# Optimization experiments

Measured on AMD Instinct MI355X. Metric: run time of the kernel, lower is better.

The kernel has to match this reference:

```python
import jax, jax.numpy as jnp
import numpy as np

B, S, C = 16, 1024, 8
V, D, E, H, R = 50257, 512, 8, 512, 32
F, RT, CD, Q = 1024, 512, 64, 128
EPS = 1e-6


def _normalize(x):
    n = jnp.maximum(jnp.linalg.norm(x, axis=-1, keepdims=True), EPS)
    return x / n


def _fake_quantize(x):
    # F.normalize then straight-through int8 quant on the unit vector
    xn = _normalize(x)
    q = jnp.clip(jnp.round(xn * 127.0), -127.0, 127.0)
    return xn + jax.lax.stop_gradient(q / 127.0 - xn)


def setup_inputs() -> dict:
    key = jax.random.key(0)
    ks = iter(jax.random.split(key, 64))

    def w(shape, s=0.02):
        return (jax.random.normal(next(ks), shape, dtype=jnp.float32) * s)

    inp = {}
    inp['prefix_tokens'] = jax.random.randint(next(ks), (B, S), 0, V, dtype=jnp.int32)
    inp['chunk_inputs'] = jax.random.randint(next(ks), (B, C), 0, V, dtype=jnp.int32)
    inp['chunk_targets'] = jax.random.randint(next(ks), (B, C), 0, V, dtype=jnp.int32)
    inp['next_chunk_tokens'] = jax.random.randint(next(ks), (B, C), 0, V, dtype=jnp.int32)

    inp['emb'] = w((V, D))
    # stacked per-expert AffineExpert params
    inp['Wa'] = w((E, D, H)); inp['ba'] = jnp.zeros((E, H), jnp.float32)
    inp['Wg'] = w((E, D, R)); inp['bg'] = jnp.zeros((E, R), jnp.float32)
    inp['Wu'] = w((E, D, H)); inp['bu'] = jnp.zeros((E, H), jnp.float32)
    inp['u_mat'] = w((E, H, R)); inp['v_mat'] = w((E, H, R))
    inp['Wp'] = w((E, H, F)); inp['bp'] = jnp.zeros((E, F), jnp.float32)
    # gate MLP
    inp['Wg1'] = w((D, D)); inp['bg1'] = jnp.zeros((D,), jnp.float32)
    inp['Wg2'] = w((D, E)); inp['bg2'] = jnp.zeros((E,), jnp.float32)
    # query / target / key / code-expansion / write-code
    inp['Wq'] = w((F, Q)); inp['bq'] = jnp.zeros((Q,), jnp.float32)
    inp['Wt1'] = w((2 * D, RT)); inp['bt1'] = jnp.zeros((RT,), jnp.float32)
    inp['Wt2'] = w((RT, RT)); inp['bt2'] = jnp.zeros((RT,), jnp.float32)
    inp['Wk'] = w((RT, Q)); inp['bk'] = jnp.zeros((Q,), jnp.float32)
    inp['Web'] = w((CD, RT))  # expansion_basis (no bias)
    inp['Wwc'] = w((F, CD)); inp['bwc'] = jnp.zeros((CD,), jnp.float32)
    # ctx MLP
    inp['Wc1'] = w((2 * F, F)); inp['bc1'] = jnp.zeros((F,), jnp.float32)
    inp['Wc2'] = w((F, F)); inp['bc2'] = jnp.zeros((F,), jnp.float32)
    # chunk decoder
    inp['chunk_pos'] = w((C, F))
    inp['Wci'] = w((D + F, F)); inp['bci'] = jnp.zeros((F,), jnp.float32)
    inp['Wm1'] = w((F, F)); inp['bm1'] = jnp.zeros((F,), jnp.float32)
    inp['Wm2'] = w((F, F)); inp['bm2'] = jnp.zeros((F,), jnp.float32)
    inp['Wlm'] = w((F, V)); inp['blm'] = jnp.zeros((V,), jnp.float32)
    return inp


def _expert_scan(x, Wa, ba, Wg, bg, Wu, bu, u_mat, v_mat):
    # x: [B,S,D]; precompute all per-step projections as one big GEMM each,
    # leading axis = time for lax.scan. A,U: [S,E,B,H], G: [S,E,B,R]
    A = jax.nn.sigmoid(jnp.einsum('bsd,edh->sebh', x, Wa) + ba[None, :, None, :])
    G = jnp.einsum('bsd,edr->sebr', x, Wg) + bg[None, :, None, :]
    U = jnp.einsum('bsd,edh->sebh', x, Wu) + bu[None, :, None, :]

    def step(state, inp):  # state: [E,B,H]
        a, g, u = inp
        low = jnp.einsum('ebh,ehr->ebr', state, v_mat) * g
        state = a * state + u + jnp.einsum('ebr,ehr->ebh', low, u_mat)
        return state, None

    state0 = jnp.zeros((E, B, H), x.dtype)
    state, _ = jax.lax.scan(step, state0, (A, G, U))
    return state  # [E,B,H]


def reference(prefix_tokens, chunk_inputs, chunk_targets, next_chunk_tokens,
              emb, Wa, ba, Wg, bg, Wu, bu, u_mat, v_mat, Wp, bp,
              Wg1, bg1, Wg2, bg2, Wq, bq, Wt1, bt1, Wt2, bt2, Wk, bk,
              Web, Wwc, bwc, Wc1, bc1, Wc2, bc2,
              chunk_pos, Wci, bci, Wm1, bm1, Wm2, bm2, Wlm, blm):
    # ---- encode_prefix ----
    prefix_emb = emb[prefix_tokens]                       # [B,S,D]
    summary = prefix_emb.mean(axis=1)                     # [B,D]
    gate_probs = jax.nn.softmax(jax.nn.silu(summary @ Wg1 + bg1) @ Wg2 + bg2, axis=-1)  # [B,E]
    states = _expert_scan(prefix_emb, Wa, ba, Wg, bg, Wu, bu, u_mat, v_mat)             # [E,B,H]
    proj = jnp.einsum('ebh,ehf->ebf', states, Wp) + bp[:, None, :]                       # [E,B,F]
    fused = jnp.einsum('ebf,be->bf', proj, gate_probs)    # [B,F]

    # ---- query / target / key ----
    q_st = _fake_quantize(fused @ Wq + bq)                # [B,Q]
    chunk_emb = emb[chunk_targets].mean(axis=1)           # [B,D]
    next_emb = emb[next_chunk_tokens].mean(axis=1)        # [B,D]
    t_in = jnp.concatenate([chunk_emb, next_emb], axis=-1)
    target_state = _normalize(jax.nn.silu(t_in @ Wt1 + bt1) @ Wt2 + bt2)  # [B,RT]
    target_k_st = _fake_quantize(target_state @ Wk + bk)  # [B,Q]

    # ---- read_context (bank=None path -> zero read) ----
    zero_read = jnp.zeros_like(fused)
    c_in = jnp.concatenate([fused, zero_read], axis=-1)
    ctx = jax.nn.silu(c_in @ Wc1 + bc1) @ Wc2 + bc2       # [B,F]

    # ---- write_from_ctx ----
    write_codes = ctx @ Wwc + bwc                         # [B,CD]
    write_state = _normalize(write_codes @ Web)           # [B,RT]
    write_k_st = _fake_quantize(write_state @ Wk + bk)    # [B,Q]

    # ---- decode_chunk ----
    tok = emb[chunk_inputs]                               # [B,C,D]
    ctx_rep = jnp.broadcast_to(ctx[:, None, :], (B, C, F))
    hidden = jnp.concatenate([tok, ctx_rep], axis=-1) @ Wci + bci + chunk_pos[None]  # [B,C,F]
    hidden = jax.nn.silu(hidden @ Wm1 + bm1) @ Wm2 + bm2
    logits = hidden @ Wlm + blm                           # [B,C,V]

    # ---- losses ----
    logp = jax.nn.log_softmax(logits, axis=-1)
    token_loss = -jnp.take_along_axis(logp, chunk_targets[..., None], axis=-1)[..., 0]
    loss_nll = token_loss.mean()
    sim = (q_st @ target_k_st.T) / jnp.sqrt(jnp.float32(Q))  # [B,B]
    return logits, loss_nll, sim, write_k_st
```

## Files before the change

### kernel.cpp

```cpp
#include <hip/hip_runtime.h>
#include <math.h>

constexpr int BB = 16;
constexpr int SS = 1024;
constexpr int CC = 8;
constexpr int VV = 50257;
constexpr int DD = 512;
constexpr int EE = 8;
constexpr int HH = 512;
constexpr int RR = 32;
constexpr int FF = 1024;
constexpr int RTd = 512;
constexpr int CDd = 64;
constexpr int QQ = 128;
constexpr int SCH = 128;

typedef short bf16x8 __attribute__((ext_vector_type(8)));
typedef float f32x4 __attribute__((ext_vector_type(4)));

__device__ __forceinline__ float sigm(float x){ return 1.0f/(1.0f+expf(-x)); }

__device__ __forceinline__ unsigned short f2bf(float f){
  unsigned int u = __float_as_uint(f);
  u += 0x7fff + ((u>>16)&1);
  return (unsigned short)(u>>16);
}
__device__ __forceinline__ float bf2f(unsigned short h){
  return __uint_as_float(((unsigned int)h)<<16);
}

__device__ __forceinline__ void gload16(unsigned short* l, const unsigned short* g){
  __builtin_amdgcn_global_load_lds(
      (const __attribute__((address_space(1))) unsigned int*)(g),
      (__attribute__((address_space(3))) unsigned int*)(l), 16, 0, 0);
}

__global__ __launch_bounds__(256) void gather_split(const int* __restrict__ toks,
    const float* __restrict__ emb,
    unsigned short* __restrict__ xh, unsigned short* __restrict__ xl){
  int idx = blockIdx.x*256 + threadIdx.x;
  int row = idx >> 7;
  int c4  = idx & 127;
  float4 v = ((const float4*)emb)[(size_t)toks[row]*128 + c4];
  float vv[4] = {v.x, v.y, v.z, v.w};
  ushort4 h, l;
  unsigned short hh[4], ll[4];
  #pragma unroll
  for (int j=0;j<4;j++){
    hh[j] = f2bf(vv[j]);
    ll[j] = f2bf(vv[j] - bf2f(hh[j]));
  }
  h = make_ushort4(hh[0],hh[1],hh[2],hh[3]);
  l = make_ushort4(ll[0],ll[1],ll[2],ll[3]);
  ((ushort4*)xh)[idx] = h;
  ((ushort4*)xl)[idx] = l;
}

__global__ __launch_bounds__(512) void colsum_part(const unsigned short* __restrict__ xh,
    const unsigned short* __restrict__ xl, float* __restrict__ part){
  int b = blockIdx.y, j = blockIdx.x, d = threadIdx.x;
  float s = 0.f;
  for (int k=0;k<64;k++){
    size_t idx = ((size_t)(b*SS) + j*64 + k)*DD + d;
    s += bf2f(xh[idx]) + bf2f(xl[idx]);
  }
  part[(b*16 + j)*DD + d] = s;
}
__global__ __launch_bounds__(512) void colsum_final(const float* __restrict__ part,
                                                    float* __restrict__ summary){
  int b = blockIdx.x, d = threadIdx.x;
  float s = 0.f;
  for (int j=0;j<16;j++) s += part[(b*16 + j)*DD + d];
  summary[b*DD + d] = s * (1.0f/1024.0f);
}

__global__ __launch_bounds__(128) void gate_h1(const float* __restrict__ summary,
                                               const float* __restrict__ Wg1,
                                               const float* __restrict__ bg1,
                                               float* __restrict__ h1){
  int t = threadIdx.x; int j = blockIdx.x*128 + t;
  __shared__ float sm[16*512];
  for (int idx=t; idx<8192; idx+=128) sm[idx] = summary[idx];
  __syncthreads();
  float acc[16] = {0};
  for (int d=0; d<DD; d++){
    float w = Wg1[d*DD + j];
    #pragma unroll
    for (int b2=0;b2<16;b2++) acc[b2] += sm[b2*DD + d]*w;
  }
  #pragma unroll
  for (int b2=0;b2<16;b2++){ float v = acc[b2] + bg1[j]; h1[b2*DD + j] = v*sigm(v); }
}
__global__ __launch_bounds__(128) void gate_probs_k(const float* __restrict__ h1,
                                                    const float* __restrict__ Wg2,
                                                    const float* __restrict__ bg2,
                                                    float* __restrict__ gate){
  int t = threadIdx.x;
  int b = t>>3, e = t&7;
  float acc = bg2[e];
  for (int d=0; d<DD; d++) acc += h1[b*DD + d]*Wg2[d*EE + e];
  __shared__ float lg[16][8];
  lg[b][e] = acc;
  __syncthreads();
  if (e==0){
    float m = -3.4e38f;
    for (int i=0;i<8;i++) m = fmaxf(m, lg[b][i]);
    float s = 0.f; float ex[8];
    for (int i=0;i<8;i++){ ex[i] = expf(lg[b][i]-m); s += ex[i]; }
    for (int i=0;i<8;i++) gate[b*EE + i] = ex[i]/s;
  }
}

__global__ __launch_bounds__(256) void convT_wl(const float* __restrict__ Wa,
    const float* __restrict__ Wu,
    unsigned short* __restrict__ WaTh, unsigned short* __restrict__ WaTl,
    unsigned short* __restrict__ WuTh, unsigned short* __restrict__ WuTl){
  int ez = blockIdx.z;
  const float* W; unsigned short *Th, *Tl;
  if (ez < 8){
    W = Wa + (size_t)ez*DD*HH; Th = WaTh + (size_t)ez*HH*DD; Tl = WaTl + (size_t)ez*HH*DD;
  } else {
    int e2 = ez-8;
    W = Wu + (size_t)e2*DD*HH; Th = WuTh + (size_t)e2*HH*DD; Tl = WuTl + (size_t)e2*HH*DD;
  }
  int k0 = blockIdx.x*64, c0 = blockIdx.y*64;
  __shared__ float tile[64][65];
  int t = threadIdx.x;
  for (int i=0;i<16;i++){
    int id = t + i*256;
    int cc = id&63, kk = id>>6;
    tile[kk][cc] = W[(size_t)(k0+kk)*HH + c0+cc];
  }
  __syncthreads();
  for (int i=0;i<16;i++){
    int id = t + i*256;
    int kk = id&63, cc = id>>6;
    float f = tile[kk][cc];
    unsigned short h = f2bf(f);
    float lo = f - bf2f(h);
    Th[(size_t)(c0+cc)*DD + k0+kk] = h;
    Tl[(size_t)(c0+cc)*DD + k0+kk] = f2bf(lo);
  }
}
__global__ __launch_bounds__(256) void convT_g(const float* __restrict__ Wge,
    unsigned short* __restrict__ WgeTh, unsigned short* __restrict__ WgeTl){
  int k0 = blockIdx.x*64, e = blockIdx.y;
  __shared__ float tile[64][33];
  int t = threadIdx.x;
  for (int i=0;i<8;i++){
    int id = t + i*256;
    int r = id&31, kk = id>>5;
    tile[kk][r] = Wge[((size_t)e*DD + k0+kk)*RR + r];
  }
  __syncthreads();
  for (int i=0;i<8;i++){
    int id = t + i*256;
    int kk = id&63, r = id>>6;
    float f = tile[kk][r];
    unsigned short h = f2bf(f);
    float lo = f - bf2f(h);
    WgeTh[(size_t)(e*RR + r)*DD + k0+kk] = h;
    WgeTl[(size_t)(e*RR + r)*DD + k0+kk] = f2bf(lo);
  }
}

__global__ __launch_bounds__(512, 4) void aug_scan(
    const unsigned short* __restrict__ xh, const unsigned short* __restrict__ xl,
    const unsigned short* __restrict__ WaTh, const unsigned short* __restrict__ WaTl,
    const unsigned short* __restrict__ WuTh, const unsigned short* __restrict__ WuTl,
    const unsigned short* __restrict__ WgeTh, const unsigned short* __restrict__ WgeTl,
    const float* __restrict__ ba, const float* __restrict__ bu, const float* __restrict__ bge,
    float* __restrict__ Aw, float* __restrict__ Uw, float* __restrict__ Gw,
    const float* __restrict__ Ar, const float* __restrict__ Ur, const float* __restrict__ Gr,
    const float* __restrict__ v_mat, const float* __restrict__ u_mat,
    float* __restrict__ states,
    int s0, int do_aug, int do_scan)
{
  __shared__ __align__(16) unsigned short lds[32768];
  const int t = threadIdx.x;

  if (blockIdx.x < 128){
    if (!do_scan) return;
    const int e = blockIdx.x >> 4;
    const int b = blockIdx.x & 15;
    const int r = t & 31, grp = t >> 5;
    float* stf   = (float*)lds;
    float* partf = (float*)lds + 1024;
    float* lowf  = (float*)lds + 1312;
    float vreg[32];
    #pragma unroll
    for (int i=0;i<32;i++) vreg[i] = v_mat[((size_t)e*HH + grp*32 + i)*RR + r];
    float ureg[32];
    {
      const float4* up = (const float4*)(u_mat + ((size_t)e*HH + t)*RR);
      #pragma unroll
      for (int j=0;j<8;j++){
        float4 v4 = up[j];
        ureg[j*4+0]=v4.x; ureg[j*4+1]=v4.y; ureg[j*4+2]=v4.z; ureg[j*4+3]=v4.w;
      }
    }
    const size_t base  = ((size_t)e*BB + b)*HH + t;
    const size_t gbase = ((size_t)e*BB + b)*RR + r;
    const size_t strAU = (size_t)EE*BB*HH;
    const size_t strG  = (size_t)EE*BB*RR;
    float streg = states[base];
    stf[t] = streg;
    float a0 = Ar[base], u0 = Ur[base];
    float g0 = (t < 32) ? Gr[gbase] : 0.f;
    float a1 = 0.f, u1 = 0.f, g1 = 0.f;
    a1 = Ar[base + strAU]; u1 = Ur[base + strAU];
    g1 = (t < 32) ? Gr[gbase + strG] : 0.f;
    __syncthreads();
    int cur = 0;
    for (int s=0; s<SCH; s++){
      float a2 = 0.f, u2 = 0.f, g2 = 0.f;
      if (s+2 < SCH){
        a2 = Ar[base + (size_t)(s+2)*strAU];
        u2 = Ur[base + (size_t)(s+2)*strAU];
        if (t < 32) g2 = Gr[gbase + (size_t)(s+2)*strG];
      }
      float p = 0.f;
      #pragma unroll
      for (int i=0;i<32;i++) p += stf[cur*512 + grp*32+i]*vreg[i];
      p += __shfl_xor(p, 32, 64);
      if ((t & 32) == 0) partf[r*9 + (grp>>1)] = p;
      __syncthreads();
      if (t < 32){
        float ss2 = 0.f;
        #pragma unroll
        for (int j=0;j<8;j++) ss2 += partf[t*9 + j];
        lowf[t] = ss2 * g0;
      }
      __syncthreads();
      float acc2 = 0.f;
      #pragma unroll
      for (int i=0;i<32;i++) acc2 += lowf[i]*ureg[i];
      streg = a0*streg + u0 + acc2;
      stf[(cur^1)*512 + t] = streg;
      cur ^= 1;
      a0=a1; u0=u1; g0=g1; a1=a2; u1=u2; g1=g2;
      __syncthreads();
    }
    states[base] = streg;
    return;
  }

  if (!do_aug) return;
  const int aid = blockIdx.x - 128;
  const int b  = aid & 15;
  const int ct = aid >> 4;
  const bool isG = (ct >= 64);
  const int lane = t & 63, wv = t >> 6;

  unsigned short* const XSH = lds;
  unsigned short* const XSL = lds + 8192;
  unsigned short* const WAH = lds + 16384;
  unsigned short* const WAL = lds + 20480;
  unsigned short* const WUH = lds + 24576;
  unsigned short* const WUL = lds + 28672;

  int e = 0, c0 = 0;
  const unsigned short* Wptr[4];
  if (!isG){
    e = ct >> 3; c0 = (ct & 7)*64;
    Wptr[0] = WaTh + ((size_t)e*HH + c0)*DD;
    Wptr[1] = WaTl + ((size_t)e*HH + c0)*DD;
    Wptr[2] = WuTh + ((size_t)e*HH + c0)*DD;
    Wptr[3] = WuTl + ((size_t)e*HH + c0)*DD;
  } else {
    c0 = (ct - 64)*64;
    Wptr[0] = WgeTh + (size_t)c0*DD;
    Wptr[1] = WgeTl + (size_t)c0*DD;
    Wptr[2] = Wptr[0]; Wptr[3] = Wptr[1];
  }
  unsigned short* const LW[4] = {WAH, WAL, WUH, WUL};
  const unsigned short* xhp = xh + ((size_t)b*SS + s0)*DD;
  const unsigned short* xlp = xl + ((size_t)b*SS + s0)*DD;

  f32x4 acc[2][4] = {};

#define STAGE(J, K0) { \
    const int wbase = (J)*512 + (t & 448); \
    const int id = wbase + lane; \
    if ((J) < 4){ \
      const int local = id & 1023; \
      const int row = local >> 3; \
      const int kq = (local & 7) ^ (row & 7); \
      const unsigned short* g = (((J) < 2) ? xhp : xlp) + (size_t)row*DD + (K0) + kq*8; \
      unsigned short* lp = (((J) < 2) ? XSH : XSL) + (wbase & 1023)*8; \
      gload16(lp, g); \
    } else { \
      const int local = id & 511; \
      const int kq = local >> 6; \
      const int c = (local & 63) ^ kq; \
      const unsigned short* g = Wptr[(J)-4] + (size_t)c*DD + (K0) + kq*8; \
      unsigned short* lp = LW[(J)-4] + (wbase & 511)*8; \
      gload16(lp, g); \
    } }

  const int strip = wv & 3;
  const int mode  = wv >> 2;
  unsigned short* const WH = mode ? WUH : WAH;
  unsigned short* const WL = mode ? WUL : WAL;

  for (int kc=0; kc<8; kc++){
    const int k0 = kc*64;
    if (kc) __syncthreads();
    STAGE(0, k0) STAGE(1, k0) STAGE(2, k0) STAGE(3, k0)
    STAGE(4, k0) STAGE(5, k0)
    if (!isG){ STAGE(6, k0) STAGE(7, k0) }
    __syncthreads();

    if (!isG){
      #pragma unroll
      for (int ks=0; ks<2; ks++){
        const int kq4 = ks*4 + (lane>>4);
        const int rr0 = strip*32 + (lane&15);
        const int rr1 = rr0 + 16;
        bf16x8 ah0 = *(const bf16x8*)&XSH[(rr0*8 + (kq4^(rr0&7)))*8];
        bf16x8 ah1 = *(const bf16x8*)&XSH[(rr1*8 + (kq4^(rr1&7)))*8];
        bf16x8 al0 = *(const bf16x8*)&XSL[(rr0*8 + (kq4^(rr0&7)))*8];
        bf16x8 al1 = *(const bf16x8*)&XSL[(rr1*8 + (kq4^(rr1&7)))*8];
        #pragma unroll
        for (int cf=0; cf<4; cf++){
          const int cc = cf*16 + (lane&15);
          bf16x8 bh = *(const bf16x8*)&WH[(kq4*64 + (cc^kq4))*8];
          bf16x8 bl = *(const bf16x8*)&WL[(kq4*64 + (cc^kq4))*8];
          acc[0][cf] = __builtin_amdgcn_mfma_f32_16x16x32_bf16(ah0, bh, acc[0][cf], 0,0,0);
          acc[0][cf] = __builtin_amdgcn_mfma_f32_16x16x32_bf16(ah0, bl, acc[0][cf], 0,0,0);
          acc[0][cf] = __builtin_amdgcn_mfma_f32_16x16x32_bf16(al0, bh, acc[0][cf], 0,0,0);
          acc[1][cf] = __builtin_amdgcn_mfma_f32_16x16x32_bf16(ah1, bh, acc[1][cf], 0,0,0);
          acc[1][cf] = __builtin_amdgcn_mfma_f32_16x16x32_bf16(ah1, bl, acc[1][cf], 0,0,0);
          acc[1][cf] = __builtin_amdgcn_mfma_f32_16x16x32_bf16(al1, bh, acc[1][cf], 0,0,0);
        }
      }
    } else {
      #pragma unroll
      for (int ks=0; ks<2; ks++){
        const int kq4 = ks*4 + (lane>>4);
        const int rr0 = wv*16 + (lane&15);
        bf16x8 ah0 = *(const bf16x8*)&XSH[(rr0*8 + (kq4^(rr0&7)))*8];
        bf16x8 al0 = *(const bf16x8*)&XSL[(rr0*8 + (kq4^(rr0&7)))*8];
        #pragma unroll
        for (int cf=0; cf<4; cf++){
          const int cc = cf*16 + (lane&15);
          bf16x8 bh = *(const bf16x8*)&WAH[(kq4*64 + (cc^kq4))*8];
          bf16x8 bl = *(const bf16x8*)&WAL[(kq4*64 + (cc^kq4))*8];
          acc[0][cf] = __builtin_amdgcn_mfma_f32_16x16x32_bf16(ah0, bh, acc[0][cf], 0,0,0);
          acc[0][cf] = __builtin_amdgcn_mfma_f32_16x16x32_bf16(ah0, bl, acc[0][cf], 0,0,0);
          acc[0][cf] = __builtin_amdgcn_mfma_f32_16x16x32_bf16(al0, bh, acc[0][cf], 0,0,0);
        }
      }
    }
  }
#undef STAGE

  const int cl = lane & 15;
  const int r4 = (lane >> 4) * 4;
  if (!isG){
    #pragma unroll
    for (int rf=0; rf<2; rf++){
      #pragma unroll
      for (int cf=0; cf<4; cf++){
        #pragma unroll
        for (int i=0;i<4;i++){
          int sl = strip*32 + rf*16 + r4 + i;
          int ce = c0 + cf*16 + cl;
          float v = acc[rf][cf][i];
          if (mode == 0){
            v += ba[e*HH + ce];
            v = sigm(v);
            Aw[((size_t)(sl*EE + e)*BB + b)*HH + ce] = v;
          } else {
            v += bu[e*HH + ce];
            Uw[((size_t)(sl*EE + e)*BB + b)*HH + ce] = v;
          }
        }
      }
    }
  } else {
    #pragma unroll
    for (int cf=0; cf<4; cf++){
      #pragma unroll
      for (int i=0;i<4;i++){
        int sl = wv*16 + r4 + i;
        int g = c0 + cf*16 + cl;
        int ee = g >> 5, r2 = g & 31;
        float v = acc[0][cf][i] + bge[ee*RR + r2];
        Gw[((size_t)(sl*EE + ee)*BB + b)*RR + r2] = v;
      }
    }
  }
}

__global__ __launch_bounds__(128) void proj_partial(const float* __restrict__ states,
    const float* __restrict__ Wp, const float* __restrict__ gate, float* __restrict__ pf){
  int fc = blockIdx.x, e = blockIdx.y, t = threadIdx.x;
  __shared__ float stl[16*512];
  for (int idx=t; idx<8192; idx+=128) stl[idx] = states[(size_t)e*8192 + idx];
  __syncthreads();
  int f = fc*128 + t;
  float acc[16] = {0};
  for (int h=0; h<HH; h++){
    float w = Wp[((size_t)e*HH + h)*FF + f];
    #pragma unroll
    for (int b2=0;b2<16;b2++) acc[b2] += stl[b2*HH + h]*w;
  }
  #pragma unroll
  for (int b2=0;b2<16;b2++) pf[((size_t)(e*16 + b2))*FF + f] = gate[b2*EE + e]*acc[b2];
}
__global__ __launch_bounds__(256) void fuse_reduce(const float* __restrict__ pf,
    const float* __restrict__ gate, const float* __restrict__ bp, float* __restrict__ fused){
  int idx = blockIdx.x*256 + threadIdx.x;
  int b = idx >> 10, f = idx & 1023;
  float s = 0.f;
  #pragma unroll
  for (int e=0;e<8;e++) s += pf[((size_t)(e*16 + b))*FF + f] + gate[b*EE + e]*bp[e*FF + f];
  fused[idx] = s;
}

__global__ __launch_bounds__(128) void fq_linear(const float* __restrict__ in, int Kin,
    const float* __restrict__ W, const float* __restrict__ bias, float* __restrict__ out){
  int b = blockIdx.x, t = threadIdx.x;
  __shared__ float xin[1024];
  __shared__ float red[2];
  for (int k=t;k<Kin;k+=128) xin[k] = in[(size_t)b*Kin + k];
  __syncthreads();
  float acc = bias[t];
  for (int k=0;k<Kin;k++) acc += xin[k]*W[k*QQ + t];
  float ss = acc*acc;
  #pragma unroll
  for (int off=32; off; off>>=1) ss += __shfl_xor(ss, off, 64);
  if ((t&63)==0) red[t>>6] = ss;
  __syncthreads();
  float n = fmaxf(sqrtf(red[0]+red[1]), 1e-6f);
  float xn = acc / n;
  float q = fminf(fmaxf(rintf(xn*127.0f), -127.0f), 127.0f) * (1.0f/127.0f);
  out[b*QQ + t] = q;
}

__global__ __launch_bounds__(512) void chunk_means(const int* __restrict__ ct,
    const int* __restrict__ nct, const float* __restrict__ emb, float* __restrict__ tin){
  int b = blockIdx.x, d = threadIdx.x;
  float ce=0.f, ne=0.f;
  for (int c=0;c<CC;c++){
    ce += emb[(size_t)ct[b*CC+c]*DD + d];
    ne += emb[(size_t)nct[b*CC+c]*DD + d];
  }
  tin[b*1024 + d] = ce*0.125f;
  tin[b*1024 + 512 + d] = ne*0.125f;
}

__global__ __launch_bounds__(512) void target_state_kernel(const float* __restrict__ tin,
    const float* __restrict__ Wt1, const float* __restrict__ bt1,
    const float* __restrict__ Wt2, const float* __restrict__ bt2, float* __restrict__ outts){
  int b = blockIdx.x, t = threadIdx.x;
  __shared__ float xin[1024];
  __shared__ float h1[512];
  __shared__ float red[8];
  for (int k=t;k<1024;k+=512) xin[k] = tin[b*1024 + k];
  __syncthreads();
  float acc = bt1[t];
  for (int k=0;k<1024;k++) acc += xin[k]*Wt1[k*RTd + t];
  acc = acc*sigm(acc);
  h1[t] = acc;
  __syncthreads();
  float y = bt2[t];
  for (int k=0;k<512;k++) y += h1[k]*Wt2[k*RTd + t];
  float ss = y*y;
// ... 205 lines not shown
  #pragma unroll
  for (int off=32; off; off>>=1){
    float m2 = __shfl_xor(m, off, 64);
    float s2 = __shfl_xor(s, off, 64);
    float mn = fmaxf(m, m2);
    s = s*expf(m - mn) + s2*expf(m2 - mn);
    m = mn;
  }
  __shared__ float ms[8], ssh[8];
  if ((t&63)==0){ ms[t>>6] = m; ssh[t>>6] = s; }
  __syncthreads();
  if (t==0){
    float M = ms[0], S = ssh[0];
    for (int i=1;i<8;i++){
      float mn = fmaxf(M, ms[i]);
      S = S*expf(M-mn) + ssh[i]*expf(ms[i]-mn);
      M = mn;
    }
    tl[row] = M + logf(S) - p[tgt[row]];
  }
}
__global__ __launch_bounds__(128) void loss_reduce(const float* __restrict__ tl,
                                                   float* __restrict__ out){
  int t = threadIdx.x;
  float v = tl[t];
  #pragma unroll
  for (int off=32; off; off>>=1) v += __shfl_xor(v, off, 64);
  __shared__ float r2[2];
  if ((t&63)==0) r2[t>>6] = v;
  __syncthreads();
  if (t==0) out[0] = (r2[0]+r2[1]) * (1.0f/128.0f);
}

extern "C" void kernel_launch(void* const* d_in, const int* in_sizes, int n_in,
                              void* d_out, int out_size, void* d_ws, size_t ws_size,
                              hipStream_t stream){
  (void)in_sizes; (void)n_in; (void)out_size;
  const int*  prefix = (const int*)d_in[0];
  const int*  cinp   = (const int*)d_in[1];
  const int*  ctgt   = (const int*)d_in[2];
  const int*  nctk   = (const int*)d_in[3];
  const float* emb  = (const float*)d_in[4];
  const float* Wa   = (const float*)d_in[5];
  const float* ba   = (const float*)d_in[6];
  const float* Wge  = (const float*)d_in[7];
  const float* bge  = (const float*)d_in[8];
  const float* Wu   = (const float*)d_in[9];
  const float* bu   = (const float*)d_in[10];
  const float* u_mat= (const float*)d_in[11];
  const float* v_mat= (const float*)d_in[12];
  const float* Wp   = (const float*)d_in[13];
  const float* bp   = (const float*)d_in[14];
  const float* Wg1  = (const float*)d_in[15];
  const float* bg1  = (const float*)d_in[16];
  const float* Wg2  = (const float*)d_in[17];
  const float* bg2  = (const float*)d_in[18];
  const float* Wq   = (const float*)d_in[19];
  const float* bq   = (const float*)d_in[20];
  const float* Wt1  = (const float*)d_in[21];
  const float* bt1  = (const float*)d_in[22];
  const float* Wt2  = (const float*)d_in[23];
  const float* bt2  = (const float*)d_in[24];
  const float* Wk   = (const float*)d_in[25];
  const float* bk   = (const float*)d_in[26];
  const float* Web  = (const float*)d_in[27];
  const float* Wwc  = (const float*)d_in[28];
  const float* bwc  = (const float*)d_in[29];
  const float* Wc1  = (const float*)d_in[30];
  const float* bc1  = (const float*)d_in[31];
  const float* Wc2  = (const float*)d_in[32];
  const float* bc2  = (const float*)d_in[33];
  const float* cpos = (const float*)d_in[34];
  const float* Wci  = (const float*)d_in[35];
  const float* bci  = (const float*)d_in[36];
  const float* Wm1  = (const float*)d_in[37];
  const float* bm1  = (const float*)d_in[38];
  const float* Wm2  = (const float*)d_in[39];
  const float* bm2  = (const float*)d_in[40];
  const float* Wlm  = (const float*)d_in[41];
  const float* blm  = (const float*)d_in[42];

  float* ws = (float*)d_ws;
  size_t off = 0;
  unsigned short* xh_all = (unsigned short*)(ws + off); off += (size_t)BB*SS*DD/2;
  unsigned short* xl_all = (unsigned short*)(ws + off); off += (size_t)BB*SS*DD/2;
  float* Abuf0  = ws + off; off += (size_t)SCH*EE*BB*HH;
  float* Ubuf0  = ws + off; off += (size_t)SCH*EE*BB*HH;
  float* Gbuf0  = ws + off; off += (size_t)SCH*EE*BB*RR;
  float* statesb= ws + off; off += (size_t)EE*BB*HH;
  float* partb  = ws + off; off += (size_t)BB*16*DD;
  float* summb  = ws + off; off += (size_t)BB*DD;
  float* h1b    = ws + off; off += (size_t)BB*DD;
  float* gateb  = ws + off; off += (size_t)BB*EE;
  float* pfb    = ws + off; off += (size_t)EE*BB*FF;
  float* fusedb = ws + off; off += (size_t)BB*FF;
  float* qstb   = ws + off; off += (size_t)BB*QQ;
  float* tinb   = ws + off; off += (size_t)BB*2*DD;
  float* tstb   = ws + off; off += (size_t)BB*RTd;
  float* tkb    = ws + off; off += (size_t)BB*QQ;
  float* ctxb   = ws + off; off += (size_t)BB*FF;
  float* hctxb  = ws + off; off += (size_t)BB*FF;
  float* wsnb   = ws + off; off += (size_t)BB*RTd;
  float* xcatb  = ws + off; off += (size_t)BB*CC*(DD+FF);
  float* hid1b  = ws + off; off += (size_t)BB*CC*FF;
  float* h2b    = ws + off; off += (size_t)BB*CC*FF;
  float* hidb   = ws + off; off += (size_t)BB*CC*FF;
  float* tlb    = ws + off; off += (size_t)BB*CC;
  float* ppart  = ws + off; off += (size_t)4*BB*CC*FF;
  unsigned short* WaTh = (unsigned short*)(ws + off); off += (size_t)EE*DD*HH/2;
  unsigned short* WaTl = (unsigned short*)(ws + off); off += (size_t)EE*DD*HH/2;
  unsigned short* WuTh = (unsigned short*)(ws + off); off += (size_t)EE*DD*HH/2;
  unsigned short* WuTl = (unsigned short*)(ws + off); off += (size_t)EE*DD*HH/2;
  unsigned short* WgeTh= (unsigned short*)(ws + off); off += (size_t)EE*DD*RR/2;
  unsigned short* WgeTl= (unsigned short*)(ws + off); off += (size_t)EE*DD*RR/2;
  unsigned short* hhb  = (unsigned short*)(ws + off); off += (size_t)BB*CC*FF/2;
  unsigned short* hlb  = (unsigned short*)(ws + off); off += (size_t)BB*CC*FF/2;
  float* Abuf1  = ws + off; off += (size_t)SCH*EE*BB*HH;
  float* Ubuf1  = ws + off; off += (size_t)SCH*EE*BB*HH;
  float* Gbuf1  = ws + off; off += (size_t)SCH*EE*BB*RR;
  const bool fused = ws_size >= off * sizeof(float);

  float* out = (float*)d_out;
  const size_t LOGITS_OFF = 0;
  const size_t LOSS_OFF = (size_t)BB*CC*VV;
  const size_t SIM_OFF  = LOSS_OFF + 1;
  const size_t WK_OFF   = SIM_OFF + (size_t)BB*BB;

  convT_wl<<<dim3(8,8,16), 256, 0, stream>>>(Wa, Wu, WaTh, WaTl, WuTh, WuTl);
  convT_g<<<dim3(8,8), 256, 0, stream>>>(Wge, WgeTh, WgeTl);

  gather_split<<<8192, 256, 0, stream>>>(prefix, emb, xh_all, xl_all);
  colsum_part<<<dim3(16,16), 512, 0, stream>>>(xh_all, xl_all, partb);
  colsum_final<<<16, 512, 0, stream>>>(partb, summb);
  gate_h1<<<4, 128, 0, stream>>>(summb, Wg1, bg1, h1b);
  gate_probs_k<<<1, 128, 0, stream>>>(h1b, Wg2, bg2, gateb);

  hipMemsetAsync(statesb, 0, (size_t)EE*BB*HH*sizeof(float), stream);

  if (fused){
    for (int c=0; c<=8; c++){
      int da = (c<8) ? 1 : 0;
      int dscn = (c>=1) ? 1 : 0;
      float* Aw = (c&1) ? Abuf1 : Abuf0;
      float* Uw = (c&1) ? Ubuf1 : Ubuf0;
      float* Gw = (c&1) ? Gbuf1 : Gbuf0;
      const float* Ar = ((c-1)&1) ? Abuf1 : Abuf0;
      const float* Ur = ((c-1)&1) ? Ubuf1 : Ubuf0;
      const float* Gr = ((c-1)&1) ? Gbuf1 : Gbuf0;
      int grid = da ? 1216 : 128;
      aug_scan<<<grid, 512, 0, stream>>>(xh_all, xl_all,
          WaTh, WaTl, WuTh, WuTl, WgeTh, WgeTl, ba, bu, bge,
          Aw, Uw, Gw, Ar, Ur, Gr, v_mat, u_mat, statesb,
          c*SCH, da, dscn);
    }
  } else {
    for (int c=0; c<8; c++){
      aug_scan<<<1216, 512, 0, stream>>>(xh_all, xl_all,
          WaTh, WaTl, WuTh, WuTl, WgeTh, WgeTl, ba, bu, bge,
          Abuf0, Ubuf0, Gbuf0, Abuf0, Ubuf0, Gbuf0, v_mat, u_mat, statesb,
          c*SCH, 1, 0);
      aug_scan<<<128, 512, 0, stream>>>(xh_all, xl_all,
          WaTh, WaTl, WuTh, WuTl, WgeTh, WgeTl, ba, bu, bge,
          Abuf0, Ubuf0, Gbuf0, Abuf0, Ubuf0, Gbuf0, v_mat, u_mat, statesb,
          c*SCH, 0, 1);
    }
  }

  proj_partial<<<dim3(8,8), 128, 0, stream>>>(statesb, Wp, gateb, pfb);
  fuse_reduce<<<64, 256, 0, stream>>>(pfb, gateb, bp, fusedb);

  fq_linear<<<16, 128, 0, stream>>>(fusedb, FF, Wq, bq, qstb);
  chunk_means<<<16, 512, 0, stream>>>(ctgt, nctk, emb, tinb);
  target_state_kernel<<<16, 512, 0, stream>>>(tinb, Wt1, bt1, Wt2, bt2, tstb);
  fq_linear<<<16, 128, 0, stream>>>(tstb, RTd, Wk, bk, tkb);

  gemm_part<<<dim3(16,1,4), 256, 0, stream>>>(fusedb, Wc1, ppart, FF, 4, 16);
  gemm_combine<<<64, 256, 0, stream>>>(ppart, bc1, nullptr, hctxb, 4, 16, 1);
  gemm_part<<<dim3(16,1,4), 256, 0, stream>>>(hctxb, Wc2, ppart, FF, 4, 16);
  gemm_combine<<<64, 256, 0, stream>>>(ppart, bc2, nullptr, ctxb, 4, 16, 0);

  write_state_kernel<<<16, 512, 0, stream>>>(ctxb, Wwc, bwc, Web, wsnb);
  fq_linear<<<16, 128, 0, stream>>>(wsnb, RTd, Wk, bk, out + WK_OFF);
  sim_kernel<<<1, 256, 0, stream>>>(qstb, tkb, out + SIM_OFF);

  build_xcat<<<768, 256, 0, stream>>>(cinp, emb, ctxb, xcatb);
  gemm_part<<<dim3(16,8,4), 256, 0, stream>>>(xcatb, Wci, ppart, DD+FF, 4, 128);
  gemm_combine<<<512, 256, 0, stream>>>(ppart, bci, cpos, hid1b, 4, 128, 0);
  gemm_part<<<dim3(16,8,4), 256, 0, stream>>>(hid1b, Wm1, ppart, FF, 4, 128);
  gemm_combine<<<512, 256, 0, stream>>>(ppart, bm1, nullptr, h2b, 4, 128, 1);
  gemm_part<<<dim3(16,8,4), 256, 0, stream>>>(h2b, Wm2, ppart, FF, 4, 128);
  gemm_combine<<<512, 256, 0, stream>>>(ppart, bm2, nullptr, hidb, 4, 128, 0);

  split_h<<<512, 256, 0, stream>>>(hidb, hhb, hlb);
  logits_mfma<<<(VV+63)/64, 256, 0, stream>>>(hhb, hlb, Wlm, blm, out + LOGITS_OFF);

  softmax_nll<<<BB*CC, 512, 0, stream>>>(out + LOGITS_OFF, ctgt, tlb);
  loss_reduce<<<1, 128, 0, stream>>>(tlb, out + LOSS_OFF);
}
```

Before: 1.818 ms.

## Pre-pack activations and weights into MFMA tile order with double-buffered LDS staging

After: 1.611 ms (median of 3 runs). 11.4% less time.

```diff
diff --git a/kernel.cpp b/kernel.cpp
--- a/kernel.cpp
+++ b/kernel.cpp
@@ -35,34 +35,39 @@
       (__attribute__((address_space(3))) unsigned int*)(l), 16, 0, 0);
 }
 
-__global__ __launch_bounds__(256) void gather_split(const int* __restrict__ toks,
-    const float* __restrict__ emb,
-    unsigned short* __restrict__ xh, unsigned short* __restrict__ xl){
-  int idx = blockIdx.x*256 + threadIdx.x;
-  int row = idx >> 7;
-  int c4  = idx & 127;
-  float4 v = ((const float4*)emb)[(size_t)toks[row]*128 + c4];
-  float vv[4] = {v.x, v.y, v.z, v.w};
-  ushort4 h, l;
-  unsigned short hh[4], ll[4];
-  #pragma unroll
-  for (int j=0;j<4;j++){
-    hh[j] = f2bf(vv[j]);
-    ll[j] = f2bf(vv[j] - bf2f(hh[j]));
-  }
-  h = make_ushort4(hh[0],hh[1],hh[2],hh[3]);
-  l = make_ushort4(ll[0],ll[1],ll[2],ll[3]);
-  ((ushort4*)xh)[idx] = h;
-  ((ushort4*)xl)[idx] = l;
-}
-
-__global__ __launch_bounds__(512) void colsum_part(const unsigned short* __restrict__ xh,
-    const unsigned short* __restrict__ xl, float* __restrict__ part){
+__global__ __launch_bounds__(256) void gather_pack(const int* __restrict__ toks,
+    const float* __restrict__ emb, unsigned short* __restrict__ xp){
+  int id = blockIdx.x*256 + threadIdx.x;
+  int b = id >> 17;
+  int rem = id & 131071;
+  int c = rem >> 14;
+  int rem2 = rem & 16383;
+  int kc = rem2 >> 10;
+  int pb = rem2 & 1023;
+  int row = pb >> 3, q = pb & 7;
+  int v = q ^ (row & 7);
+  int kq = v >> 1, h = v & 1;
+  int tok = toks[b*SS + c*128 + row];
+  const float* src = emb + (size_t)tok*DD + kc*32 + kq*8;
+  unsigned short o[8];
+  #pragma unroll
+  for (int j=0;j<8;j++){
+    float f = src[j];
+    unsigned short hi = f2bf(f);
+    o[j] = h ? f2bf(f - bf2f(hi)) : hi;
+  }
+  ushort4* dst = (ushort4*)(xp + (size_t)id*8);
+  dst[0] = make_ushort4(o[0],o[1],o[2],o[3]);
+  dst[1] = make_ushort4(o[4],o[5],o[6],o[7]);
+}
+
+__global__ __launch_bounds__(512) void colsum_part(const int* __restrict__ toks,
+    const float* __restrict__ emb, float* __restrict__ part){
   int b = blockIdx.y, j = blockIdx.x, d = threadIdx.x;
   float s = 0.f;
   for (int k=0;k<64;k++){
-    size_t idx = ((size_t)(b*SS) + j*64 + k)*DD + d;
-    s += bf2f(xh[idx]) + bf2f(xl[idx]);
+    int tok = toks[b*SS + j*64 + k];
+    s += emb[(size_t)tok*DD + d];
   }
   part[(b*16 + j)*DD + d] = s;
 }
@@ -111,64 +116,72 @@
   }
 }
 
-__global__ __launch_bounds__(256) void convT_wl(const float* __restrict__ Wa,
-    const float* __restrict__ Wu,
-    unsigned short* __restrict__ WaTh, unsigned short* __restrict__ WaTl,
-    unsigned short* __restrict__ WuTh, unsigned short* __restrict__ WuTl){
-  int ez = blockIdx.z;
-  const float* W; unsigned short *Th, *Tl;
-  if (ez < 8){
-    W = Wa + (size_t)ez*DD*HH; Th = WaTh + (size_t)ez*HH*DD; Tl = WaTl + (size_t)ez*HH*DD;
-  } else {
-    int e2 = ez-8;
-    W = Wu + (size_t)e2*DD*HH; Th = WuTh + (size_t)e2*HH*DD; Tl = WuTl + (size_t)e2*HH*DD;
-  }
-  int k0 = blockIdx.x*64, c0 = blockIdx.y*64;
-  __shared__ float tile[64][65];
-  int t = threadIdx.x;
-  for (int i=0;i<16;i++){
-    int id = t + i*256;
-    int cc = id&63, kk = id>>6;
-    tile[kk][cc] = W[(size_t)(k0+kk)*HH + c0+cc];
-  }
-  __syncthreads();
-  for (int i=0;i<16;i++){
-    int id = t + i*256;
-    int kk = id&63, cc = id>>6;
-    float f = tile[kk][cc];
-    unsigned short h = f2bf(f);
-    float lo = f - bf2f(h);
-    Th[(size_t)(c0+cc)*DD + k0+kk] = h;
-    Tl[(size_t)(c0+cc)*DD + k0+kk] = f2bf(lo);
-  }
-}
-__global__ __launch_bounds__(256) void convT_g(const float* __restrict__ Wge,
-    unsigned short* __restrict__ WgeTh, unsigned short* __restrict__ WgeTl){
-  int k0 = blockIdx.x*64, e = blockIdx.y;
-  __shared__ float tile[64][33];
-  int t = threadIdx.x;
+__global__ __launch_bounds__(256) void convT_pack_au(const float* __restrict__ Wa,
+    const float* __restrict__ Wu, unsigned short* __restrict__ WPackAU){
+  const int ec = blockIdx.x;
+  const int kc = blockIdx.y;
+  const int e = ec >> 3, ct = ec & 7;
+  __shared__ float ta[32][64];
+  __shared__ float tu[32][64];
+  const int t = threadIdx.x;
   for (int i=0;i<8;i++){
     int id = t + i*256;
-    int r = id&31, kk = id>>5;
-    tile[kk][r] = Wge[((size_t)e*DD + k0+kk)*RR + r];
-  }
-  __syncthreads();
+    int c = id & 63, kk = id >> 6;
+    size_t src = ((size_t)e*DD + kc*32 + kk)*HH + ct*64 + c;
+    ta[kk][c] = Wa[src];
+    tu[kk][c] = Wu[src];
+  }
+  __syncthreads();
+  unsigned short* o = WPackAU + ((size_t)ec*16 + kc)*8192;
+  for (int i=0;i<8;i++){
+    int idx4 = t + i*256;
+    int blk = idx4 >> 1, half = idx4 & 1;
+    int a = blk >> 8, kq = (blk >> 6) & 3, c = blk & 63;
+    const float* src = (a >> 1) ? &tu[0][0] : &ta[0][0];
+    unsigned short s4[4];
+    #pragma unroll
+    for (int j2=0;j2<4;j2++){
+      int j = half*4 + j2;
+      float f = src[(kq*8 + j)*64 + c];
+      unsigned short hi = f2bf(f);
+      s4[j2] = (a & 1) ? f2bf(f - bf2f(hi)) : hi;
+    }
+    *(ushort4*)&o[(size_t)idx4*4] = make_ushort4(s4[0],s4[1],s4[2],s4[3]);
+  }
+}
+__global__ __launch_bounds__(256) void convT_pack_g(const float* __restrict__ Wge,
+    unsigned short* __restrict__ WPackG){
+  const int gt = blockIdx.x;
+  const int kc = blockIdx.y;
+  __shared__ float tg[32][64];
+  const int t = threadIdx.x;
   for (int i=0;i<8;i++){
     int id = t + i*256;
-    int kk = id&63, r = id>>6;
-    float f = tile[kk][r];
-    unsigned short h = f2bf(f);
-    float lo = f - bf2f(h);
-    WgeTh[(size_t)(e*RR + r)*DD + k0+kk] = h;
-    WgeTl[(size_t)(e*RR + r)*DD + k0+kk] = f2bf(lo);
-  }
-}
-
-__global__ __launch_bounds__(512, 4) void aug_scan(
-    const unsigned short* __restrict__ xh, const unsigned short* __restrict__ xl,
-    const unsigned short* __restrict__ WaTh, const unsigned short* __restrict__ WaTl,
-    const unsigned short* __restrict__ WuTh, const unsigned short* __restrict__ WuTl,
-    const unsigned short* __restrict__ WgeTh, const unsigned short* __restrict__ WgeTl,
+    int c = id & 63, kk = id >> 6;
+    int gcol = gt*64 + c;
+    tg[kk][c] = Wge[((size_t)(gcol>>5)*DD + kc*32 + kk)*RR + (gcol & 31)];
+  }
+  __syncthreads();
+  unsigned short* o = WPackG + ((size_t)gt*16 + kc)*4096;
+  for (int i=0;i<4;i++){
+    int idx4 = t + i*256;
+    int blk = idx4 >> 1, half = idx4 & 1;
+    int a = blk >> 8, kq = (blk >> 6) & 3, c = blk & 63;
+    unsigned short s4[4];
+    #pragma unroll
+    for (int j2=0;j2<4;j2++){
+      int j = half*4 + j2;
+      float f = tg[kq*8 + j][c];
+      unsigned short hi = f2bf(f);
+      s4[j2] = a ? f2bf(f - bf2f(hi)) : hi;
+    }
+    *(ushort4*)&o[(size_t)idx4*4] = make_ushort4(s4[0],s4[1],s4[2],s4[3]);
+  }
+}
+
+__global__ __launch_bounds__(512, 2) void aug_scan(
+    const unsigned short* __restrict__ xp,
+    const unsigned short* __restrict__ WPackAU, const unsigned short* __restrict__ WPackG,
     const float* __restrict__ ba, const float* __restrict__ bu, const float* __restrict__ bge,
     float* __restrict__ Aw, float* __restrict__ Uw, float* __restrict__ Gw,
     const float* __restrict__ Ar, const float* __restrict__ Ur, const float* __restrict__ Gr,
@@ -207,9 +220,8 @@
     stf[t] = streg;
     float a0 = Ar[base], u0 = Ur[base];
     float g0 = (t < 32) ? Gr[gbase] : 0.f;
-    float a1 = 0.f, u1 = 0.f, g1 = 0.f;
-    a1 = Ar[base + strAU]; u1 = Ur[base + strAU];
-    g1 = (t < 32) ? Gr[gbase + strG] : 0.f;
+    float a1 = Ar[base + strAU], u1 = Ur[base + strAU];
+    float g1 = (t < 32) ? Gr[gbase + strG] : 0.f;
     __syncthreads();
     int cur = 0;
     for (int s=0; s<SCH; s++){
@@ -249,115 +261,69 @@
   const int aid = blockIdx.x - 128;
   const int b  = aid & 15;
   const int ct = aid >> 4;
-  const bool isG = (ct >= 64);
   const int lane = t & 63, wv = t >> 6;
-
-  unsigned short* const XSH = lds;
-  unsigned short* const XSL = lds + 8192;
-  unsigned short* const WAH = lds + 16384;
-  unsigned short* const WAL = lds + 20480;
-  unsigned short* const WUH = lds + 24576;
-  unsigned short* const WUL = lds + 28672;
-
-  int e = 0, c0 = 0;
-  const unsigned short* Wptr[4];
-  if (!isG){
-    e = ct >> 3; c0 = (ct & 7)*64;
-    Wptr[0] = WaTh + ((size_t)e*HH + c0)*DD;
-    Wptr[1] = WaTl + ((size_t)e*HH + c0)*DD;
-    Wptr[2] = WuTh + ((size_t)e*HH + c0)*DD;
-    Wptr[3] = WuTl + ((size_t)e*HH + c0)*DD;
-  } else {
-    c0 = (ct - 64)*64;
-    Wptr[0] = WgeTh + (size_t)c0*DD;
-    Wptr[1] = WgeTl + (size_t)c0*DD;
-    Wptr[2] = Wptr[0]; Wptr[3] = Wptr[1];
-  }
-  unsigned short* const LW[4] = {WAH, WAL, WUH, WUL};
-  const unsigned short* xhp = xh + ((size_t)b*SS + s0)*DD;
-  const unsigned short* xlp = xl + ((size_t)b*SS + s0)*DD;
+  const int cix = s0 >> 7;
+  const unsigned short* xpc = xp + (((size_t)(b*8 + cix)) << 17);
+  const int wo = wv*64;
 
   f32x4 acc[2][4] = {};
-
-#define STAGE(J, K0) { \
-    const int wbase = (J)*512 + (t & 448); \
-    const int id = wbase + lane; \
-    if ((J) < 4){ \
-      const int local = id & 1023; \
-      const int row = local >> 3; \
-      const int kq = (local & 7) ^ (row & 7); \
-      const unsigned short* g = (((J) < 2) ? xhp : xlp) + (size_t)row*DD + (K0) + kq*8; \
-      unsigned short* lp = (((J) < 2) ? XSH : XSL) + (wbase & 1023)*8; \
-      gload16(lp, g); \
-    } else { \
-      const int local = id & 511; \
-      const int kq = local >> 6; \
-      const int c = (local & 63) ^ kq; \
-      const unsigned short* g = Wptr[(J)-4] + (size_t)c*DD + (K0) + kq*8; \
-      unsigned short* lp = LW[(J)-4] + (wbase & 511)*8; \
-      gload16(lp, g); \
-    } }
-
-  const int strip = wv & 3;
-  const int mode  = wv >> 2;
-  unsigned short* const WH = mode ? WUH : WAH;
-  unsigned short* const WL = mode ? WUL : WAL;
-
-  for (int kc=0; kc<8; kc++){
-    const int k0 = kc*64;
-    if (kc) __syncthreads();
-    STAGE(0, k0) STAGE(1, k0) STAGE(2, k0) STAGE(3, k0)
-    STAGE(4, k0) STAGE(5, k0)
-    if (!isG){ STAGE(6, k0) STAGE(7, k0) }
-    __syncthreads();
-
-    if (!isG){
-      #pragma unroll
-      for (int ks=0; ks<2; ks++){
-        const int kq4 = ks*4 + (lane>>4);
-        const int rr0 = strip*32 + (lane&15);
-        const int rr1 = rr0 + 16;
-        bf16x8 ah0 = *(const bf16x8*)&XSH[(rr0*8 + (kq4^(rr0&7)))*8];
-        bf16x8 ah1 = *(const bf16x8*)&XSH[(rr1*8 + (kq4^(rr1&7)))*8];
-        bf16x8 al0 = *(const bf16x8*)&XSL[(rr0*8 + (kq4^(rr0&7)))*8];
-        bf16x8 al1 = *(const bf16x8*)&XSL[(rr1*8 + (kq4^(rr1&7)))*8];
-        #pragma unroll
-        for (int cf=0; cf<4; cf++){
-          const int cc = cf*16 + (lane&15);
-          bf16x8 bh = *(const bf16x8*)&WH[(kq4*64 + (cc^kq4))*8];
-          bf16x8 bl = *(const bf16x8*)&WL[(kq4*64 + (cc^kq4))*8];
-          acc[0][cf] = __builtin_amdgcn_mfma_f32_16x16x32_bf16(ah0, bh, acc[0][cf], 0,0,0);
-          acc[0][cf] = __builtin_amdgcn_mfma_f32_16x16x32_bf16(ah0, bl, acc[0][cf], 0,0,0);
-          acc[0][cf] = __builtin_amdgcn_mfma_f32_16x16x32_bf16(al0, bh, acc[0][cf], 0,0,0);
-          acc[1][cf] = __builtin_amdgcn_mfma_f32_16x16x32_bf16(ah1, bh, acc[1][cf], 0,0,0);
-          acc[1][cf] = __builtin_amdgcn_mfma_f32_16x16x32_bf16(ah1, bl, acc[1][cf], 0,0,0);
-          acc[1][cf] = __builtin_amdgcn_mfma_f32_16x16x32_bf16(al1, bh, acc[1][cf], 0,0,0);
-        }
-      }
-    } else {
-      #pragma unroll
-      for (int ks=0; ks<2; ks++){
-        const int kq4 = ks*4 + (lane>>4);
-        const int rr0 = wv*16 + (lane&15);
-        bf16x8 ah0 = *(const bf16x8*)&XSH[(rr0*8 + (kq4^(rr0&7)))*8];
-        bf16x8 al0 = *(const bf16x8*)&XSL[(rr0*8 + (kq4^(rr0&7)))*8];
-        #pragma unroll
-        for (int cf=0; cf<4; cf++){
-          const int cc = cf*16 + (lane&15);
-          bf16x8 bh = *(const bf16x8*)&WAH[(kq4*64 + (cc^kq4))*8];
-          bf16x8 bl = *(const bf16x8*)&WAL[(kq4*64 + (cc^kq4))*8];
-          acc[0][cf] = __builtin_amdgcn_mfma_f32_16x16x32_bf16(ah0, bh, acc[0][cf], 0,0,0);
-          acc[0][cf] = __builtin_amdgcn_mfma_f32_16x16x32_bf16(ah0, bl, acc[0][cf], 0,0,0);
-          acc[0][cf] = __builtin_amdgcn_mfma_f32_16x16x32_bf16(al0, bh, acc[0][cf], 0,0,0);
-        }
-      }
-    }
-  }
-#undef STAGE
-
-  const int cl = lane & 15;
-  const int r4 = (lane >> 4) * 4;
-  if (!isG){
+  const int cl15 = lane & 15;
+
+  if (ct < 64){
+    const int e = ct >> 3;
+    const int c0 = (ct & 7)*64;
+    const unsigned short* wpc = WPackAU + (((size_t)ct) << 17);
+    const int strip = wv & 3;
+    const int mode  = wv >> 2;
+    const int kq4 = lane >> 4;
+    const int rr0 = strip*32 + cl15, rr1 = rr0 + 16;
+    const int qh = (kq4*2) ^ (rr0 & 7);
+    const int ql = (kq4*2+1) ^ (rr0 & 7);
+    const int ab = mode*512;
+
+#define STAGE_AU(BUF, KC) { \
+    unsigned short* XB_ = lds + (BUF)*16384; \
+    unsigned short* WB_ = XB_ + 8192; \
+    const unsigned short* gx = xpc + (KC)*8192; \
+    const unsigned short* gw = wpc + (KC)*8192; \
+    gload16(XB_ + wo*8,        gx + (size_t)(wo + lane)*8); \
+    gload16(XB_ + (512+wo)*8,  gx + (size_t)(512 + wo + lane)*8); \
+    gload16(WB_ + wo*8,        gw + (size_t)(wo + lane)*8); \
+    gload16(WB_ + (512+wo)*8,  gw + (size_t)(512 + wo + lane)*8); }
+
+    STAGE_AU(0, 0)
+    asm volatile("s_waitcnt vmcnt(0)" ::: "memory");
+    __builtin_amdgcn_s_barrier();
+    __builtin_amdgcn_sched_barrier(0);
+    int cur = 0;
+    for (int kc=0; kc<16; kc++){
+      if (kc < 15) STAGE_AU(cur^1, kc+1)
+      const unsigned short* XB = lds + cur*16384;
+      const unsigned short* WB = XB + 8192;
+      bf16x8 ah0 = *(const bf16x8*)&XB[(rr0*8 + qh)*8];
+      bf16x8 al0 = *(const bf16x8*)&XB[(rr0*8 + ql)*8];
+      bf16x8 ah1 = *(const bf16x8*)&XB[(rr1*8 + qh)*8];
+      bf16x8 al1 = *(const bf16x8*)&XB[(rr1*8 + ql)*8];
+      #pragma unroll
+      for (int cf=0; cf<4; cf++){
+        const int cc = cf*16 + cl15;
+        bf16x8 bh = *(const bf16x8*)&WB[(ab + kq4*64 + cc)*8];
+        bf16x8 bl = *(const bf16x8*)&WB[(ab + 256 + kq4*64 + cc)*8];
+        acc[0][cf] = __builtin_amdgcn_mfma_f32_16x16x32_bf16(ah0, bh, acc[0][cf], 0,0,0);
+        acc[0][cf] = __builtin_amdgcn_mfma_f32_16x16x32_bf16(ah0, bl, acc[0][cf], 0,0,0);
+        acc[0][cf] = __builtin_amdgcn_mfma_f32_16x16x32_bf16(al0, bh, acc[0][cf], 0,0,0);
+        acc[1][cf] = __builtin_amdgcn_mfma_f32_16x16x32_bf16(ah1, bh, acc[1][cf], 0,0,0);
+        acc[1][cf] = __builtin_amdgcn_mfma_f32_16x16x32_bf16(ah1, bl, acc[1][cf], 0,0,0);
+        acc[1][cf] = __builtin_amdgcn_mfma_f32_16x16x32_bf16(al1, bh, acc[1][cf], 0,0,0);
+      }
+      __builtin_amdgcn_sched_barrier(0);
+      asm volatile("s_waitcnt vmcnt(0)" ::: "memory");
+      __builtin_amdgcn_s_barrier();
+      __builtin_amdgcn_sched_barrier(0);
+      cur ^= 1;
+    }
+#undef STAGE_AU
+    const int r4 = (lane >> 4) * 4;
     #pragma unroll
     for (int rf=0; rf<2; rf++){
       #pragma unroll
@@ -365,7 +331,7 @@
         #pragma unroll
         for (int i=0;i<4;i++){
           int sl = strip*32 + rf*16 + r4 + i;
-          int ce = c0 + cf*16 + cl;
+          int ce = c0 + cf*16 + cl15;
           float v = acc[rf][cf][i];
           if (mode == 0){
             v += ba[e*HH + ce];
@@ -379,12 +345,57 @@
       }
     }
   } else {
+    const int gt = ct - 64;
+    const int c0 = gt*64;
+    const unsigned short* wpc = WPackG + (((size_t)gt) << 16);
+    const int kq4 = lane >> 4;
+    const int rr0 = wv*16 + cl15;
+    const int qh = (kq4*2) ^ (rr0 & 7);
+    const int ql = (kq4*2+1) ^ (rr0 & 7);
+
+#define STAGE_G(BUF, KC) { \
+    unsigned short* XB_ = lds + (BUF)*16384; \
+    unsigned short* WB_ = XB_ + 8192; \
+    const unsigned short* gx = xpc + (KC)*8192; \
+    const unsigned short* gw = wpc + (KC)*4096; \
+    gload16(XB_ + wo*8,        gx + (size_t)(wo + lane)*8); \
+    gload16(XB_ + (512+wo)*8,  gx + (size_t)(512 + wo + lane)*8); \
+    gload16(WB_ + wo*8,        gw + (size_t)(wo + lane)*8); }
+
+    STAGE_G(0, 0)
+    asm volatile("s_waitcnt vmcnt(0)" ::: "memory");
+    __builtin_amdgcn_s_barrier();
+    __builtin_amdgcn_sched_barrier(0);
+    int cur = 0;
+    for (int kc=0; kc<16; kc++){
+      if (kc < 15) STAGE_G(cur^1, kc+1)
+      const unsigned short* XB = lds + cur*16384;
+      const unsigned short* WB = XB + 8192;
+      bf16x8 ah0 = *(const bf16x8*)&XB[(rr0*8 + qh)*8];
+      bf16x8 al0 = *(const bf16x8*)&XB[(rr0*8 + ql)*8];
+      #pragma unroll
+      for (int cf=0; cf<4; cf++){
+        const int cc = cf*16 + cl15;
+        bf16x8 bh = *(const bf16x8*)&WB[(kq4*64 + cc)*8];
+        bf16x8 bl = *(const bf16x8*)&WB[(256 + kq4*64 + cc)*8];
+        acc[0][cf] = __builtin_amdgcn_mfma_f32_16x16x32_bf16(ah0, bh, acc[0][cf], 0,0,0);
+        acc[0][cf] = __builtin_amdgcn_mfma_f32_16x16x32_bf16(ah0, bl, acc[0][cf], 0,0,0);
+        acc[0][cf] = __builtin_amdgcn_mfma_f32_16x16x32_bf16(al0, bh, acc[0][cf], 0,0,0);
+      }
+      __builtin_amdgcn_sched_barrier(0);
+      asm volatile("s_waitcnt vmcnt(0)" ::: "memory");
+      __builtin_amdgcn_s_barrier();
+      __builtin_amdgcn_sched_barrier(0);
+      cur ^= 1;
+    }
+#undef STAGE_G
+    const int r4 = (lane >> 4) * 4;
     #pragma unroll
     for (int cf=0; cf<4; cf++){
       #pragma unroll
       for (int i=0;i<4;i++){
         int sl = wv*16 + r4 + i;
-        int g = c0 + cf*16 + cl;
+        int g = c0 + cf*16 + cl15;
         int ee = g >> 5, r2 = g & 31;
         float v = acc[0][cf][i] + bge[ee*RR + r2];
         Gw[((size_t)(sl*EE + ee)*BB + b)*RR + r2] = v;
@@ -756,8 +767,7 @@
 
   float* ws = (float*)d_ws;
   size_t off = 0;
-  unsigned short* xh_all = (unsigned short*)(ws + off); off += (size_t)BB*SS*DD/2;
-  unsigned short* xl_all = (unsigned short*)(ws + off); off += (size_t)BB*SS*DD/2;
+  unsigned short* xp = (unsigned short*)(ws + off); off += (size_t)BB*SS*DD;
   float* Abuf0  = ws + off; off += (size_t)SCH*EE*BB*HH;
   float* Ubuf0  = ws + off; off += (size_t)SCH*EE*BB*HH;
   float* Gbuf0  = ws + off; off += (size_t)SCH*EE*BB*RR;
@@ -781,12 +791,8 @@
   float* hidb   = ws + off; off += (size_t)BB*CC*FF;
   float* tlb    = ws + off; off += (size_t)BB*CC;
   float* ppart  = ws + off; off += (size_t)4*BB*CC*FF;
-  unsigned short* WaTh = (unsigned short*)(ws + off); off += (size_t)EE*DD*HH/2;
-  unsigned short* WaTl = (unsigned short*)(ws + off); off += (size_t)EE*DD*HH/2;
-  unsigned short* WuTh = (unsigned short*)(ws + off); off += (size_t)EE*DD*HH/2;
-  unsigned short* WuTl = (unsigned short*)(ws + off); off += (size_t)EE*DD*HH/2;
-  unsigned short* WgeTh= (unsigned short*)(ws + off); off += (size_t)EE*DD*RR/2;
-  unsigned short* WgeTl= (unsigned short*)(ws + off); off += (size_t)EE*DD*RR/2;
+  unsigned short* WPackAU = (unsigned short*)(ws + off); off += (size_t)EE*DD*HH*2;
+  unsigned short* WPackG  = (unsigned short*)(ws + off); off += (size_t)EE*DD*RR;
   unsigned short* hhb  = (unsigned short*)(ws + off); off += (size_t)BB*CC*FF/2;
   unsigned short* hlb  = (unsigned short*)(ws + off); off += (size_t)BB*CC*FF/2;
   float* Abuf1  = ws + off; off += (size_t)SCH*EE*BB*HH;
@@ -800,11 +806,11 @@
   const size_t SIM_OFF  = LOSS_OFF + 1;
   const size_t WK_OFF   = SIM_OFF + (size_t)BB*BB;
 
-  convT_wl<<<dim3(8,8,16), 256, 0, stream>>>(Wa, Wu, WaTh, WaTl, WuTh, WuTl);
-  convT_g<<<dim3(8,8), 256, 0, stream>>>(Wge, WgeTh, WgeTl);
-
-  gather_split<<<8192, 256, 0, stream>>>(prefix, emb, xh_all, xl_all);
-  colsum_part<<<dim3(16,16), 512, 0, stream>>>(xh_all, xl_all, partb);
+  convT_pack_au<<<dim3(64,16), 256, 0, stream>>>(Wa, Wu, WPackAU);
+  convT_pack_g<<<dim3(4,16), 256, 0, stream>>>(Wge, WPackG);
+
+  gather_pack<<<8192, 256, 0, stream>>>(prefix, emb, xp);
+  colsum_part<<<dim3(16,16), 512, 0, stream>>>(prefix, emb, partb);
   colsum_final<<<16, 512, 0, stream>>>(partb, summb);
   gate_h1<<<4, 128, 0, stream>>>(summb, Wg1, bg1, h1b);
   gate_probs_k<<<1, 128, 0, stream>>>(h1b, Wg2, bg2, gateb);
@@ -822,19 +828,16 @@
       const float* Ur = ((c-1)&1) ? Ubuf1 : Ubuf0;
       const float* Gr = ((c-1)&1) ? Gbuf1 : Gbuf0;
       int grid = da ? 1216 : 128;
-      aug_scan<<<grid, 512, 0, stream>>>(xh_all, xl_all,
-          WaTh, WaTl, WuTh, WuTl, WgeTh, WgeTl, ba, bu, bge,
+      aug_scan<<<grid, 512, 0, stream>>>(xp, WPackAU, WPackG, ba, bu, bge,
           Aw, Uw, Gw, Ar, Ur, Gr, v_mat, u_mat, statesb,
           c*SCH, da, dscn);
     }
   } else {
     for (int c=0; c<8; c++){
-      aug_scan<<<1216, 512, 0, stream>>>(xh_all, xl_all,
-          WaTh, WaTl, WuTh, WuTl, WgeTh, WgeTl, ba, bu, bge,
+      aug_scan<<<1216, 512, 0, stream>>>(xp, WPackAU, WPackG, ba, bu, bge,
           Abuf0, Ubuf0, Gbuf0, Abuf0, Ubuf0, Gbuf0, v_mat, u_mat, statesb,
           c*SCH, 1, 0);
-      aug_scan<<<128, 512, 0, stream>>>(xh_all, xl_all,
-          WaTh, WaTl, WuTh, WuTl, WgeTh, WgeTl, ba, bu, bge,
+      aug_scan<<<128, 512, 0, stream>>>(xp, WPackAU, WPackG, ba, bu, bge,
           Abuf0, Ubuf0, Gbuf0, Abuf0, Ubuf0, Gbuf0, v_mat, u_mat, statesb,
           c*SCH, 0, 1);
     }
```
